# Performance work log

Hardware: AMD Instinct MI355X
Metric: run time of the kernel (lower is better)

## Reference

```python
import jax, jax.numpy as jnp
import numpy as np

N_NODES = 100000
N_EDGES = 1600000
D = 64
N_LAYERS = 3  # in -> h1 -> h2 -> out
LN_EPS = 1e-5


def setup_inputs() -> dict:
    key = jax.random.key(0)
    ks = jax.random.split(key, 4)
    scale = 1.0 / np.sqrt(D)
    vert_features = jax.random.normal(ks[0], (N_NODES, D), dtype=jnp.float32)
    edges = jax.random.randint(ks[1], (N_EDGES, 2), 0, N_NODES, dtype=jnp.int64)
    W0 = jax.random.normal(ks[2], (N_LAYERS, D, D), dtype=jnp.float32) * scale
    W1 = jax.random.normal(ks[3], (N_LAYERS, D, D), dtype=jnp.float32) * scale
    b0 = jnp.zeros((N_LAYERS, D), dtype=jnp.float32)
    b1 = jnp.zeros((N_LAYERS, D), dtype=jnp.float32)
    ln_gamma = jnp.ones((N_LAYERS - 1, D), dtype=jnp.float32)
    ln_beta = jnp.zeros((N_LAYERS - 1, D), dtype=jnp.float32)
    return {"vert_features": vert_features, "edges": edges, "W0": W0, "b0": b0,
            "W1": W1, "b1": b1, "ln_gamma": ln_gamma, "ln_beta": ln_beta}


def _graph_conv(h, src, dst, deg, W0l, b0l, W1l, b1l):
    # messages from every vertex, then undirected neighbor-mean aggregation
    msg = h @ W1l + b1l                                   # [N, D]
    idx = jnp.concatenate([dst, src])                     # both directions
    val = jnp.concatenate([msg[src], msg[dst]])           # [2E, D] gather
    agg = jax.ops.segment_sum(val, idx, num_segments=N_NODES)
    agg = agg / deg[:, None]                              # normalize=True
    return h @ W0l + b0l + agg


def _layer_norm(x, gamma, beta):
    mu = jnp.mean(x, axis=-1, keepdims=True)
    var = jnp.mean(jnp.square(x - mu), axis=-1, keepdims=True)
    return (x - mu) * jax.lax.rsqrt(var + LN_EPS) * gamma + beta


def reference(vert_features, edges, W0, b0, W1, b1, ln_gamma, ln_beta):
    src = edges[:, 0]
    dst = edges[:, 1]
    idx = jnp.concatenate([dst, src])
    deg = jax.ops.segment_sum(jnp.ones((2 * N_EDGES,), jnp.float32), idx,
                              num_segments=N_NODES)
    deg = jnp.maximum(deg, 1.0)
    h = vert_features
    for l in range(N_LAYERS - 1):
        h = _graph_conv(h, src, dst, deg, W0[l], b0[l], W1[l], b1[l])
        h = _layer_norm(h, ln_gamma[l], ln_beta[l])
        h = jax.nn.relu(h)
    h = _graph_conv(h, src, dst, deg, W0[-1], b0[-1], W1[-1], b1[-1])
    return h
```

## Files before the change

kernel.cpp:

```cpp
#include <hip/hip_runtime.h>
#include <hip/hip_bf16.h>

constexpr int D_ = 64;
constexpr int NN = 100000;
constexpr int NE = 1600000;
constexpr int RB = 8;

constexpr int BUCK_SH = 7;
constexpr int NBUCK = (NN + 127) >> BUCK_SH;
constexpr int NB1 = 256;
constexpr int NQ4 = NE / 4;
constexpr int QPB = (NQ4 + NB1 - 1) / NB1;
constexpr int SCN = NBUCK * NB1;
constexpr int SCB = (SCN + 1023) / 1024;

__global__ __launch_bounds__(256) void k_s1count(const int* __restrict__ edges,
                                                 int* __restrict__ cnts) {
  __shared__ int hist[NBUCK];
  for (int i = threadIdx.x; i < NBUCK; i += 256) hist[i] = 0;
  __syncthreads();
  const int q0 = blockIdx.x * QPB;
  const int q1 = min(q0 + QPB, NQ4);
  for (int q = q0 + (int)threadIdx.x; q < q1; q += 256) {
    const int4* ep = reinterpret_cast<const int4*>(edges + 8 * q);
    int4 a = ep[0], b = ep[1];
    atomicAdd(&hist[a.x >> BUCK_SH], 1);
    atomicAdd(&hist[a.y >> BUCK_SH], 1);
    atomicAdd(&hist[a.z >> BUCK_SH], 1);
    atomicAdd(&hist[a.w >> BUCK_SH], 1);
    atomicAdd(&hist[b.x >> BUCK_SH], 1);
    atomicAdd(&hist[b.y >> BUCK_SH], 1);
    atomicAdd(&hist[b.z >> BUCK_SH], 1);
    atomicAdd(&hist[b.w >> BUCK_SH], 1);
  }
  __syncthreads();
  for (int i = threadIdx.x; i < NBUCK; i += 256)
    cnts[i * NB1 + blockIdx.x] = hist[i];
}

__global__ __launch_bounds__(1024) void k_scanA(const int* __restrict__ cnt,
                                                int* __restrict__ oscan,
                                                int* __restrict__ bsum, int n) {
  __shared__ int sd[1024];
  const int tid = threadIdx.x;
  const int i = blockIdx.x * 1024 + tid;
  int v = (i < n) ? cnt[i] : 0;
  sd[tid] = v;
  __syncthreads();
  for (int off = 1; off < 1024; off <<= 1) {
    int t = (tid >= off) ? sd[tid - off] : 0;
    __syncthreads();
    sd[tid] += t;
    __syncthreads();
  }
  if (i < n) oscan[i] = sd[tid] - v;
  if (tid == 1023) bsum[blockIdx.x] = sd[1023];
}

__global__ __launch_bounds__(256) void k_scanB(int* __restrict__ bsum, int nb) {
  __shared__ int sd[256];
  const int tid = threadIdx.x;
  int v = (tid < nb) ? bsum[tid] : 0;
  sd[tid] = v;
  __syncthreads();
  for (int off = 1; off < 256; off <<= 1) {
    int t = (tid >= off) ? sd[tid - off] : 0;
    __syncthreads();
    sd[tid] += t;
    __syncthreads();
  }
  if (tid < nb) bsum[tid] = sd[tid] - v;
}

__global__ __launch_bounds__(256) void k_scanC(int* __restrict__ oscan,
                                               const int* __restrict__ bsum, int n) {
  int i = blockIdx.x * 256 + threadIdx.x;
  if (i < n) oscan[i] += bsum[i >> 10];
}

__global__ __launch_bounds__(256) void k_s1scatter(const int* __restrict__ edges,
                                                   const int* __restrict__ sscan,
                                                   unsigned* __restrict__ items) {
  __shared__ int cur[NBUCK];
  for (int i = threadIdx.x; i < NBUCK; i += 256)
    cur[i] = sscan[i * NB1 + blockIdx.x];
  __syncthreads();
  const int q0 = blockIdx.x * QPB;
  const int q1 = min(q0 + QPB, NQ4);
  for (int q = q0 + (int)threadIdx.x; q < q1; q += 256) {
    const int4* ep = reinterpret_cast<const int4*>(edges + 8 * q);
    int4 a = ep[0], b = ep[1];
    int p;
    p = atomicAdd(&cur[a.y >> BUCK_SH], 1); items[p] = ((unsigned)(a.y & 127) << 17) | (unsigned)a.x;
    p = atomicAdd(&cur[a.x >> BUCK_SH], 1); items[p] = ((unsigned)(a.x & 127) << 17) | (unsigned)a.y;
    p = atomicAdd(&cur[a.w >> BUCK_SH], 1); items[p] = ((unsigned)(a.w & 127) << 17) | (unsigned)a.z;
    p = atomicAdd(&cur[a.z >> BUCK_SH], 1); items[p] = ((unsigned)(a.z & 127) << 17) | (unsigned)a.w;
    p = atomicAdd(&cur[b.y >> BUCK_SH], 1); items[p] = ((unsigned)(b.y & 127) << 17) | (unsigned)b.x;
    p = atomicAdd(&cur[b.x >> BUCK_SH], 1); items[p] = ((unsigned)(b.x & 127) << 17) | (unsigned)b.y;
    p = atomicAdd(&cur[b.w >> BUCK_SH], 1); items[p] = ((unsigned)(b.w & 127) << 17) | (unsigned)b.z;
    p = atomicAdd(&cur[b.z >> BUCK_SH], 1); items[p] = ((unsigned)(b.z & 127) << 17) | (unsigned)b.w;
  }
}

__global__ __launch_bounds__(256) void k_s2build(const unsigned* __restrict__ items,
                                                 const int* __restrict__ sscan,
                                                 int* __restrict__ offs,
                                                 int* __restrict__ nbr) {
  const int b = blockIdx.x;
  const int lo = b << BUCK_SH;
  __shared__ int hist[128], scn[128];
  __shared__ int sbase, send;
  if (threadIdx.x == 0) {
    sbase = sscan[b * NB1];
    send = (b + 1 < NBUCK) ? sscan[(b + 1) * NB1] : 2 * NE;
  }
  if (threadIdx.x < 128) hist[threadIdx.x] = 0;
  __syncthreads();
  const int i0 = sbase, i1 = send;
  for (int i = i0 + (int)threadIdx.x; i < i1; i += 256)
    atomicAdd(&hist[items[i] >> 17], 1);
  __syncthreads();
  if (threadIdx.x < 128) scn[threadIdx.x] = hist[threadIdx.x];
  __syncthreads();
  for (int off = 1; off < 128; off <<= 1) {
    int t = (threadIdx.x < 128 && (int)threadIdx.x >= off) ? scn[threadIdx.x - off] : 0;
    __syncthreads();
    if (threadIdx.x < 128) scn[threadIdx.x] += t;
    __syncthreads();
  }
  if (threadIdx.x < 128) {
    int node = lo + threadIdx.x;
    int ex = sbase + scn[threadIdx.x] - hist[threadIdx.x];
    if (node < NN) offs[node] = ex;
    hist[threadIdx.x] = ex;
  }
  __syncthreads();
  for (int i = i0 + (int)threadIdx.x; i < i1; i += 256) {
    unsigned it = items[i];
    int pos = atomicAdd(&hist[it >> 17], 1);
    nbr[pos] = (int)(it & 0x1FFFFu);
  }
  if (b == 0 && threadIdx.x == 0) offs[NN] = 2 * NE;
}

__device__ __forceinline__ void stage_w_pk(const float* __restrict__ W0,
                                           const float* __restrict__ W1,
                                           unsigned* wP) {
  for (int i = threadIdx.x; i < 4096; i += 256) {
    int k = i >> 6, j = i & 63;
    wP[j * 68 + k] = (__float_as_uint(W1[i]) & 0xffff0000u) |
                     (__float_as_uint(W0[i]) >> 16);
  }
}

__device__ __forceinline__ unsigned char f32_to_f8(float v) {
  return (unsigned char)(__builtin_amdgcn_cvt_pk_fp8_f32(v, v, 0, false) & 0xff);
}

#define ACC8(mvv)                                                   \
  do {                                                              \
    auto lo = __builtin_amdgcn_cvt_pk_f32_fp8((mvv), false);        \
    auto hi = __builtin_amdgcn_cvt_pk_f32_fp8((mvv), true);         \
    acc[0] += lo[0]; acc[1] += lo[1]; acc[2] += hi[0]; acc[3] += hi[1]; \
  } while (0)

__device__ __forceinline__ float gather_row_q8(const unsigned* __restrict__ msgu,
                                               const int* __restrict__ nbr,
                                               int n0, int n1, int q, int c,
                                               int lane) {
  float acc[4] = {0.0f, 0.0f, 0.0f, 0.0f};
  int jb = n0;
  if (jb + 32 <= n1) {
    int idx[8];
#pragma unroll
    for (int u = 0; u < 8; ++u) idx[u] = nbr[jb + 4 * u + q];
    for (;;) {
      unsigned mv[8];
#pragma unroll
      for (int u = 0; u < 8; ++u) mv[u] = msgu[(idx[u] << 4) + c];
      const int jn = jb + 32;
      const bool more = (jn + 32 <= n1);
      if (more) {
#pragma unroll
        for (int u = 0; u < 8; ++u) idx[u] = nbr[jn + 4 * u + q];
      }
#pragma unroll
      for (int u = 0; u < 8; ++u) ACC8(mv[u]);
      jb = jn;
      if (!more) break;
    }
  }
  if (jb + 16 <= n1) {
    int idx[4];
#pragma unroll
    for (int u = 0; u < 4; ++u) idx[u] = nbr[jb + 4 * u + q];
    unsigned mv[4];
#pragma unroll
    for (int u = 0; u < 4; ++u) mv[u] = msgu[(idx[u] << 4) + c];
#pragma unroll
    for (int u = 0; u < 4; ++u) ACC8(mv[u]);
    jb += 16;
  }
  if (jb + 8 <= n1) {
    int i0 = nbr[jb + q], i1 = nbr[jb + 4 + q];
    unsigned m0 = msgu[(i0 << 4) + c];
    unsigned m1 = msgu[(i1 << 4) + c];
    ACC8(m0);
    ACC8(m1);
    jb += 8;
  }
  if (jb < n1) {
    int i0 = nbr[min(jb + q, n1 - 1)];
    int i1 = nbr[min(jb + 4 + q, n1 - 1)];
    unsigned m0 = msgu[(i0 << 4) + c];
    unsigned m1 = msgu[(i1 << 4) + c];
    if (jb + q >= n1) m0 = 0u;
    if (jb + 4 + q >= n1) m1 = 0u;
    ACC8(m0);
    ACC8(m1);
  }
#pragma unroll
  for (int k = 0; k < 4; ++k) {
    acc[k] += __shfl_xor(acc[k], 16, 64);
    acc[k] += __shfl_xor(acc[k], 32, 64);
  }
  float t0 = __shfl(acc[0], lane >> 2, 64);
  float t1 = __shfl(acc[1], lane >> 2, 64);
  float t2 = __shfl(acc[2], lane >> 2, 64);
  float t3 = __shfl(acc[3], lane >> 2, 64);
  const int s = lane & 3;
  return (s == 0) ? t0 : ((s == 1) ? t1 : ((s == 2) ? t2 : t3));
}

__device__ __forceinline__ void gemm_batch(const unsigned* wP,
                                           const float* myrows, int lane,
                                           float bv0, float bv1,
                                           float* a0, float* a1) {
#pragma unroll
  for (int rr = 0; rr < RB; ++rr) { a0[rr] = bv0; a1[rr] = bv1; }
#pragma unroll 1
  for (int k4 = 0; k4 < 16; ++k4) {
    uint4 up = *reinterpret_cast<const uint4*>(&wP[lane * 68 + k4 * 4]);
    const float v0x = __uint_as_float(up.x << 16);
    const float v1x = __uint_as_float(up.x & 0xffff0000u);
    const float v0y = __uint_as_float(up.y << 16);
    const float v1y = __uint_as_float(up.y & 0xffff0000u);
    const float v0z = __uint_as_float(up.z << 16);
    const float v1z = __uint_as_float(up.z & 0xffff0000u);
    const float v0w = __uint_as_float(up.w << 16);
    const float v1w = __uint_as_float(up.w & 0xffff0000u);
#pragma unroll
    for (int rr = 0; rr < RB; ++rr) {
      float4 hv = *reinterpret_cast<const float4*>(&myrows[rr * 64 + k4 * 4]);
      a0[rr] = fmaf(hv.x, v0x, a0[rr]); a1[rr] = fmaf(hv.x, v1x, a1[rr]);
      a0[rr] = fmaf(hv.y, v0y, a0[rr]); a1[rr] = fmaf(hv.y, v1y, a1[rr]);
      a0[rr] = fmaf(hv.z, v0z, a0[rr]); a1[rr] = fmaf(hv.z, v1z, a1[rr]);
      a0[rr] = fmaf(hv.w, v0w, a0[rr]); a1[rr] = fmaf(hv.w, v1w, a1[rr]);
    }
  }
}

__global__ __launch_bounds__(256) void k_gemm2(
    const float* __restrict__ h, const float* __restrict__ W0,
    const float* __restrict__ b0, const float* __restrict__ W1,
    const float* __restrict__ b1, float* __restrict__ base,
    unsigned char* __restrict__ msg, int nrows) {
  __shared__ unsigned wP[64 * 68];
  __shared__ float rbuf[4][RB * 64];
  stage_w_pk(W0, W1, wP);
  __syncthreads();
  const int lane = threadIdx.x & 63;
  const int wv = threadIdx.x >> 6;
  const int wid = (blockIdx.x * 256 + threadIdx.x) >> 6;
  const int nw = (gridDim.x * 256) >> 6;
  const float bv0 = b0[lane], bv1 = b1[lane];
  float* myrows = rbuf[wv];

  const int chunk = (nrows + nw - 1) / nw;
  const int r0 = wid * chunk;
  const int r1 = min(r0 + chunk, nrows);
  if (r0 >= nrows) return;

  float st[RB];
#pragma unroll
  for (int rr = 0; rr < RB; ++rr) {
    int r = min(r0 + rr, nrows - 1);
    st[rr] = h[(size_t)r * 64 + lane];
  }
  for (int rb = r0; rb < r1; rb += RB) {
#pragma unroll
    for (int rr = 0; rr < RB; ++rr) myrows[rr * 64 + lane] = st[rr];
    const int nb = rb + RB;
    if (nb < r1) {
#pragma unroll
      for (int rr = 0; rr < RB; ++rr) {
        int r = min(nb + rr, nrows - 1);
        st[rr] = h[(size_t)r * 64 + lane];
      }
    }
    float a0[RB], a1[RB];
    gemm_batch(wP, myrows, lane, bv0, bv1, a0, a1);
#pragma unroll
    for (int rr = 0; rr < RB; ++rr) {
      int r = rb + rr;
      if (r < r1) {
        base[(size_t)r * 64 + lane] = a0[rr];
        msg[(size_t)r * 64 + lane] = f32_to_f8(a1[rr]);
      }
    }
  }
}

__global__ __launch_bounds__(256) void k_fused(
    float* __restrict__ base, const unsigned char* __restrict__ msgin,
    unsigned char* __restrict__ msgout,
    const int* __restrict__ offs, const int* __restrict__ nbr,
    const float* __restrict__ gamma, const float* __restrict__ beta,
    const float* __restrict__ W0n, const float* __restrict__ b0n,
    const float* __restrict__ W1n, const float* __restrict__ b1n, int nrows) {
  __shared__ unsigned wP[64 * 68];
  __shared__ float rbuf[4][RB * 64];
  stage_w_pk(W0n, W1n, wP);
  __syncthreads();
  const int lane = threadIdx.x & 63;
  const int wv = threadIdx.x >> 6;
  const int q = lane >> 4;
  const int c = lane & 15;
  const int wid = (blockIdx.x * 256 + threadIdx.x) >> 6;
  const int nw = (gridDim.x * 256) >> 6;
  const float gm = gamma[lane], bt = beta[lane];
  const float bv0 = b0n[lane], bv1 = b1n[lane];
  float* myrows = rbuf[wv];
  const unsigned* msgu = reinterpret_cast<const unsigned*>(msgin);

  const int chunk = (nrows + nw - 1) / nw;
  const int r0 = wid * chunk;
  const int r1 = min(r0 + chunk, nrows);
  if (r0 >= nrows) return;

  for (int rb = r0; rb < r1; rb += RB) {
#pragma unroll 1
    for (int rr = 0; rr < RB; ++rr) {
      int r = rb + rr;
      if (r >= r1) break;
      const int n0 = offs[r], n1 = offs[r + 1];
      const float bval = base[(size_t)r * 64 + lane];
      float ag = gather_row_q8(msgu, nbr, n0, n1, q, c, lane);
      const float rdeg = 1.0f / fmaxf((float)(n1 - n0), 1.0f);
      float val = fmaf(ag, rdeg, bval);
      float s = val, s2 = val * val;
#pragma unroll
      for (int off = 32; off > 0; off >>= 1) {
        s += __shfl_xor(s, off, 64);
        s2 += __shfl_xor(s2, off, 64);
      }
      const float mu = s * (1.0f / 64.0f);
      const float var = fmaxf(s2 * (1.0f / 64.0f) - mu * mu, 0.0f);
      const float dv = val - mu;
      val = fmaxf(fmaf(dv * rsqrtf(var + 1e-5f), gm, bt), 0.0f);
      myrows[rr * 64 + lane] = val;
    }
    float a0[RB], a1[RB];
    gemm_batch(wP, myrows, lane, bv0, bv1, a0, a1);
#pragma unroll
    for (int rr = 0; rr < RB; ++rr) {
      int r = rb + rr;
      if (r < r1) {
        base[(size_t)r * 64 + lane] = a0[rr];
        msgout[(size_t)r * 64 + lane] = f32_to_f8(a1[rr]);
      }
    }
  }
}

__global__ __launch_bounds__(256) void k_aggF(
    float* __restrict__ base, const unsigned char* __restrict__ msg,
    const int* __restrict__ offs, const int* __restrict__ nbr, int nrows) {
  const int lane = threadIdx.x & 63;
  const int q = lane >> 4;
  const int c = lane & 15;
  const int wid = (blockIdx.x * 256 + threadIdx.x) >> 6;
  const int nw = (gridDim.x * 256) >> 6;
  const unsigned* msgu = reinterpret_cast<const unsigned*>(msg);
  for (int r = wid; r < nrows; r += nw) {
    const int n0 = offs[r], n1 = offs[r + 1];
    const float bval = base[(size_t)r * 64 + lane];
    float ag = gather_row_q8(msgu, nbr, n0, n1, q, c, lane);
    const float rdeg = 1.0f / fmaxf((float)(n1 - n0), 1.0f);
    base[(size_t)r * 64 + lane] = fmaf(ag, rdeg, bval);
  }
}

extern "C" void kernel_launch(void* const* d_in, const int* in_sizes, int n_in,
                              void* d_out, int out_size, void* d_ws, size_t ws_size,
                              hipStream_t stream) {
  const float* vert = (const float*)d_in[0];
  const int* edges = (const int*)d_in[1];
  const float* W0 = (const float*)d_in[2];
  const float* b0 = (const float*)d_in[3];
  const float* W1 = (const float*)d_in[4];
  const float* b1 = (const float*)d_in[5];
  const float* lng = (const float*)d_in[6];
  const float* lnb = (const float*)d_in[7];
  float* base = (float*)d_out;

  const size_t NBR_B = (size_t)2 * NE * 4;
  const size_t MSG_B = (size_t)NN * 64;
  int* nbr = (int*)d_ws;
  char* creg = (char*)d_ws + NBR_B;
  unsigned* items = (unsigned*)creg;
  unsigned char* msgA = (unsigned char*)creg;
  unsigned char* msgB = (unsigned char*)(creg + MSG_B);
  int* offs = (int*)(creg + NBR_B);
  int* cnts = (int*)d_out;
  int* sscan = cnts + SCN;
  int* bsum = sscan + SCN;

  k_s1count<<<NB1, 256, 0, stream>>>(edges, cnts);
  k_scanA<<<SCB, 1024, 0, stream>>>(cnts, sscan, bsum, SCN);
  k_scanB<<<1, 256, 0, stream>>>(bsum, SCB);
  k_scanC<<<(SCN + 255) / 256, 256, 0, stream>>>(sscan, bsum, SCN);
  k_s1scatter<<<NB1, 256, 0, stream>>>(edges, sscan, items);
  k_s2build<<<NBUCK, 256, 0, stream>>>(items, sscan, offs, nbr);

  const int GG = 1536;
  const int GF = 1536;
  const int GA = 2048;

  k_gemm2<<<GG, 256, 0, stream>>>(vert, W0, b0, W1, b1, base, msgA, NN);
  k_fused<<<GF, 256, 0, stream>>>(base, msgA, msgB, offs, nbr,
                                  lng, lnb, W0 + 4096, b0 + 64,
                                  W1 + 4096, b1 + 64, NN);
  k_fused<<<GF, 256, 0, stream>>>(base, msgB, msgA, offs, nbr,
                                  lng + 64, lnb + 64, W0 + 8192, b0 + 128,
                                  W1 + 8192, b1 + 128, NN);
  k_aggF<<<GA, 256, 0, stream>>>(base, msgA, offs, nbr, NN);
}
```

Measured before the change: 373.6 us.

## Gather neighbor messages for four rows at once per wavefront

Replaces the single-row neighbor gather with a gather4 routine. It walks the adjacency lists of four rows together, issuing up to 16 independent index and message loads per step. The goal is more memory-level parallelism, to hide the latency of the random fp8 message gathers in both the fused LN+GEMM kernel and the final aggregation kernel. The final aggregation kernel also switches from strided to contiguous per-wave row chunks. In exchange, each group loops until its highest-degree row is done, with masked loads, and register pressure rises from the 4x4 accumulators.

```diff
diff --git a/kernel.cpp b/kernel.cpp
--- a/kernel.cpp
+++ b/kernel.cpp
@@ -157,79 +157,72 @@
   return (unsigned char)(__builtin_amdgcn_cvt_pk_fp8_f32(v, v, 0, false) & 0xff);
 }
 
-#define ACC8(mvv)                                                   \
-  do {                                                              \
-    auto lo = __builtin_amdgcn_cvt_pk_f32_fp8((mvv), false);        \
-    auto hi = __builtin_amdgcn_cvt_pk_f32_fp8((mvv), true);         \
-    acc[0] += lo[0]; acc[1] += lo[1]; acc[2] += hi[0]; acc[3] += hi[1]; \
-  } while (0)
-
-__device__ __forceinline__ float gather_row_q8(const unsigned* __restrict__ msgu,
-                                               const int* __restrict__ nbr,
-                                               int n0, int n1, int q, int c,
-                                               int lane) {
-  float acc[4] = {0.0f, 0.0f, 0.0f, 0.0f};
-  int jb = n0;
-  if (jb + 32 <= n1) {
-    int idx[8];
-#pragma unroll
-    for (int u = 0; u < 8; ++u) idx[u] = nbr[jb + 4 * u + q];
-    for (;;) {
-      unsigned mv[8];
-#pragma unroll
-      for (int u = 0; u < 8; ++u) mv[u] = msgu[(idx[u] << 4) + c];
-      const int jn = jb + 32;
-      const bool more = (jn + 32 <= n1);
-      if (more) {
-#pragma unroll
-        for (int u = 0; u < 8; ++u) idx[u] = nbr[jn + 4 * u + q];
-      }
-#pragma unroll
-      for (int u = 0; u < 8; ++u) ACC8(mv[u]);
-      jb = jn;
-      if (!more) break;
-    }
-  }
-  if (jb + 16 <= n1) {
-    int idx[4];
-#pragma unroll
-    for (int u = 0; u < 4; ++u) idx[u] = nbr[jb + 4 * u + q];
-    unsigned mv[4];
-#pragma unroll
-    for (int u = 0; u < 4; ++u) mv[u] = msgu[(idx[u] << 4) + c];
-#pragma unroll
-    for (int u = 0; u < 4; ++u) ACC8(mv[u]);
-    jb += 16;
-  }
-  if (jb + 8 <= n1) {
-    int i0 = nbr[jb + q], i1 = nbr[jb + 4 + q];
-    unsigned m0 = msgu[(i0 << 4) + c];
-    unsigned m1 = msgu[(i1 << 4) + c];
-    ACC8(m0);
-    ACC8(m1);
-    jb += 8;
-  }
-  if (jb < n1) {
-    int i0 = nbr[min(jb + q, n1 - 1)];
-    int i1 = nbr[min(jb + 4 + q, n1 - 1)];
-    unsigned m0 = msgu[(i0 << 4) + c];
-    unsigned m1 = msgu[(i1 << 4) + c];
-    if (jb + q >= n1) m0 = 0u;
-    if (jb + 4 + q >= n1) m1 = 0u;
-    ACC8(m0);
-    ACC8(m1);
-  }
-#pragma unroll
-  for (int k = 0; k < 4; ++k) {
-    acc[k] += __shfl_xor(acc[k], 16, 64);
-    acc[k] += __shfl_xor(acc[k], 32, 64);
-  }
-  float t0 = __shfl(acc[0], lane >> 2, 64);
-  float t1 = __shfl(acc[1], lane >> 2, 64);
-  float t2 = __shfl(acc[2], lane >> 2, 64);
-  float t3 = __shfl(acc[3], lane >> 2, 64);
-  const int s = lane & 3;
-  return (s == 0) ? t0 : ((s == 1) ? t1 : ((s == 2) ? t2 : t3));
+__device__ __forceinline__ void gather4(const unsigned* __restrict__ msgu,
+                                        const int* __restrict__ nbr,
+                                        const int* __restrict__ offs,
+                                        int rbase, int rclamp,
+                                        int q, int c, int lane,
+                                        float* __restrict__ val,
+                                        float* __restrict__ rdeg) {
+  int n1[4], jb[4];
+#pragma unroll
+  for (int i = 0; i < 4; ++i) {
+    int r = min(rbase + i, rclamp);
+    jb[i] = offs[r];
+    n1[i] = offs[r + 1];
+    rdeg[i] = 1.0f / fmaxf((float)(n1[i] - jb[i]), 1.0f);
+  }
+  float acc[4][4];
+#pragma unroll
+  for (int i = 0; i < 4; ++i)
+#pragma unroll
+    for (int k = 0; k < 4; ++k) acc[i][k] = 0.0f;
+  bool any = (jb[0] < n1[0]) | (jb[1] < n1[1]) | (jb[2] < n1[2]) | (jb[3] < n1[3]);
+  while (any) {
+    unsigned mv[4][4];
+#pragma unroll
+    for (int i = 0; i < 4; ++i) {
+      if (jb[i] < n1[i]) {
+#pragma unroll
+        for (int u = 0; u < 4; ++u) {
+          int id = nbr[min(jb[i] + 4 * u + q, n1[i] - 1)];
+          mv[i][u] = msgu[(id << 4) + c];
+        }
+      }
+    }
+#pragma unroll
+    for (int i = 0; i < 4; ++i) {
+      if (jb[i] < n1[i]) {
+#pragma unroll
+        for (int u = 0; u < 4; ++u) {
+          unsigned m = (jb[i] + 4 * u + q < n1[i]) ? mv[i][u] : 0u;
+          auto lo = __builtin_amdgcn_cvt_pk_f32_fp8(m, false);
+          auto hi = __builtin_amdgcn_cvt_pk_f32_fp8(m, true);
+          acc[i][0] += lo[0]; acc[i][1] += lo[1];
+          acc[i][2] += hi[0]; acc[i][3] += hi[1];
+        }
+      }
+    }
+    any = false;
+#pragma unroll
+    for (int i = 0; i < 4; ++i) { jb[i] += 16; any = any | (jb[i] < n1[i]); }
+  }
+#pragma unroll
+  for (int i = 0; i < 4; ++i)
+#pragma unroll
+    for (int k = 0; k < 4; ++k) {
+      acc[i][k] += __shfl_xor(acc[i][k], 16, 64);
+      acc[i][k] += __shfl_xor(acc[i][k], 32, 64);
+    }
+#pragma unroll
+  for (int i = 0; i < 4; ++i) {
+    float t0 = __shfl(acc[i][0], lane >> 2, 64);
+    float t1 = __shfl(acc[i][1], lane >> 2, 64);
+    float t2 = __shfl(acc[i][2], lane >> 2, 64);
+    float t3 = __shfl(acc[i][3], lane >> 2, 64);
+    const int s = lane & 3;
+    val[i] = (s == 0) ? t0 : ((s == 1) ? t1 : ((s == 2) ? t2 : t3));
+  }
 }
 
 __device__ __forceinline__ void gemm_batch(const unsigned* wP,
@@ -339,26 +332,37 @@
   if (r0 >= nrows) return;
 
   for (int rb = r0; rb < r1; rb += RB) {
-#pragma unroll 1
-    for (int rr = 0; rr < RB; ++rr) {
-      int r = rb + rr;
-      if (r >= r1) break;
-      const int n0 = offs[r], n1 = offs[r + 1];
-      const float bval = base[(size_t)r * 64 + lane];
-      float ag = gather_row_q8(msgu, nbr, n0, n1, q, c, lane);
-      const float rdeg = 1.0f / fmaxf((float)(n1 - n0), 1.0f);
-      float val = fmaf(ag, rdeg, bval);
-      float s = val, s2 = val * val;
+#pragma unroll
+    for (int g = 0; g < 2; ++g) {
+      const int gb = rb + g * 4;
+      float bv4[4];
+#pragma unroll
+      for (int i = 0; i < 4; ++i)
+        bv4[i] = base[(size_t)min(gb + i, nrows - 1) * 64 + lane];
+      float v4[4], rd4[4];
+      gather4(msgu, nbr, offs, gb, nrows - 1, q, c, lane, v4, rd4);
+      float vals[4];
+#pragma unroll
+      for (int i = 0; i < 4; ++i) vals[i] = fmaf(v4[i], rd4[i], bv4[i]);
+      float sA[4], sB[4];
+#pragma unroll
+      for (int i = 0; i < 4; ++i) { sA[i] = vals[i]; sB[i] = vals[i] * vals[i]; }
 #pragma unroll
       for (int off = 32; off > 0; off >>= 1) {
-        s += __shfl_xor(s, off, 64);
-        s2 += __shfl_xor(s2, off, 64);
-      }
-      const float mu = s * (1.0f / 64.0f);
-      const float var = fmaxf(s2 * (1.0f / 64.0f) - mu * mu, 0.0f);
-      const float dv = val - mu;
-      val = fmaxf(fmaf(dv * rsqrtf(var + 1e-5f), gm, bt), 0.0f);
-      myrows[rr * 64 + lane] = val;
+#pragma unroll
+        for (int i = 0; i < 4; ++i) {
+          sA[i] += __shfl_xor(sA[i], off, 64);
+          sB[i] += __shfl_xor(sB[i], off, 64);
+        }
+      }
+#pragma unroll
+      for (int i = 0; i < 4; ++i) {
+        const float mu = sA[i] * (1.0f / 64.0f);
+        const float var = fmaxf(sB[i] * (1.0f / 64.0f) - mu * mu, 0.0f);
+        const float dv = vals[i] - mu;
+        const float o = fmaxf(fmaf(dv * rsqrtf(var + 1e-5f), gm, bt), 0.0f);
+        myrows[(g * 4 + i) * 64 + lane] = o;
+      }
     }
     float a0[RB], a1[RB];
     gemm_batch(wP, myrows, lane, bv0, bv1, a0, a1);
@@ -382,12 +386,23 @@
   const int wid = (blockIdx.x * 256 + threadIdx.x) >> 6;
   const int nw = (gridDim.x * 256) >> 6;
   const unsigned* msgu = reinterpret_cast<const unsigned*>(msg);
-  for (int r = wid; r < nrows; r += nw) {
-    const int n0 = offs[r], n1 = offs[r + 1];
-    const float bval = base[(size_t)r * 64 + lane];
-    float ag = gather_row_q8(msgu, nbr, n0, n1, q, c, lane);
-    const float rdeg = 1.0f / fmaxf((float)(n1 - n0), 1.0f);
-    base[(size_t)r * 64 + lane] = fmaf(ag, rdeg, bval);
+  const int chunk = (((nrows + nw - 1) / nw) + 3) & ~3;
+  const int r0 = wid * chunk;
+  const int r1 = min(r0 + chunk, nrows);
+  if (r0 >= nrows) return;
+  for (int rb = r0; rb < r1; rb += 4) {
+    float bv4[4];
+#pragma unroll
+    for (int i = 0; i < 4; ++i)
+      bv4[i] = base[(size_t)min(rb + i, nrows - 1) * 64 + lane];
+    float v4[4], rd4[4];
+    gather4(msgu, nbr, offs, rb, nrows - 1, q, c, lane, v4, rd4);
+#pragma unroll
+    for (int i = 0; i < 4; ++i) {
+      int r = rb + i;
+      if (r < r1)
+        base[(size_t)r * 64 + lane] = fmaf(v4[i], rd4[i], bv4[i]);
+    }
   }
 }
 
```

Result: slower. 452.5 us (+21.1%).

## Split fused aggregate+LN+GEMM kernel into separate aggregate-LN and GEMM kernels

Applied to the files above, without the earlier changes.

Replaces the fused per-layer kernel (gather aggregation, layernorm, relu, then a shared-memory GEMM for the next layer) with two kernels: a gather+layernorm kernel that writes an fp32 hidden buffer, followed by the existing standalone GEMM kernel. The aim is to decouple the irregular, latency-bound gather from the GEMM so each kernel gets its own occupancy and work split. The fused kernel also carried shared-memory weight staging and a contiguous per-wave row chunking. The split costs an extra 25.6 MB round trip for the hidden activations and two more launches per run.

```diff
diff --git a/kernel.cpp b/kernel.cpp
--- a/kernel.cpp
+++ b/kernel.cpp
@@ -311,65 +311,35 @@
   }
 }
 
-__global__ __launch_bounds__(256) void k_fused(
-    float* __restrict__ base, const unsigned char* __restrict__ msgin,
-    unsigned char* __restrict__ msgout,
+__global__ __launch_bounds__(256) void k_aggLN(
+    const float* __restrict__ base, const unsigned char* __restrict__ msg,
     const int* __restrict__ offs, const int* __restrict__ nbr,
     const float* __restrict__ gamma, const float* __restrict__ beta,
-    const float* __restrict__ W0n, const float* __restrict__ b0n,
-    const float* __restrict__ W1n, const float* __restrict__ b1n, int nrows) {
-  __shared__ unsigned wP[64 * 68];
-  __shared__ float rbuf[4][RB * 64];
-  stage_w_pk(W0n, W1n, wP);
-  __syncthreads();
+    float* __restrict__ hout, int nrows) {
   const int lane = threadIdx.x & 63;
-  const int wv = threadIdx.x >> 6;
   const int q = lane >> 4;
   const int c = lane & 15;
   const int wid = (blockIdx.x * 256 + threadIdx.x) >> 6;
   const int nw = (gridDim.x * 256) >> 6;
   const float gm = gamma[lane], bt = beta[lane];
-  const float bv0 = b0n[lane], bv1 = b1n[lane];
-  float* myrows = rbuf[wv];
-  const unsigned* msgu = reinterpret_cast<const unsigned*>(msgin);
-
-  const int chunk = (nrows + nw - 1) / nw;
-  const int r0 = wid * chunk;
-  const int r1 = min(r0 + chunk, nrows);
-  if (r0 >= nrows) return;
-
-  for (int rb = r0; rb < r1; rb += RB) {
-#pragma unroll 1
-    for (int rr = 0; rr < RB; ++rr) {
-      int r = rb + rr;
-      if (r >= r1) break;
-      const int n0 = offs[r], n1 = offs[r + 1];
-      const float bval = base[(size_t)r * 64 + lane];
-      float ag = gather_row_q8(msgu, nbr, n0, n1, q, c, lane);
-      const float rdeg = 1.0f / fmaxf((float)(n1 - n0), 1.0f);
-      float val = fmaf(ag, rdeg, bval);
-      float s = val, s2 = val * val;
-#pragma unroll
-      for (int off = 32; off > 0; off >>= 1) {
-        s += __shfl_xor(s, off, 64);
-        s2 += __shfl_xor(s2, off, 64);
-      }
-      const float mu = s * (1.0f / 64.0f);
-      const float var = fmaxf(s2 * (1.0f / 64.0f) - mu * mu, 0.0f);
-      const float dv = val - mu;
-      val = fmaxf(fmaf(dv * rsqrtf(var + 1e-5f), gm, bt), 0.0f);
-      myrows[rr * 64 + lane] = val;
+  const unsigned* msgu = reinterpret_cast<const unsigned*>(msg);
+  for (int r = wid; r < nrows; r += nw) {
+    const int n0 = offs[r], n1 = offs[r + 1];
+    const float bval = base[(size_t)r * 64 + lane];
+    float ag = gather_row_q8(msgu, nbr, n0, n1, q, c, lane);
+    const float rdeg = 1.0f / fmaxf((float)(n1 - n0), 1.0f);
+    float val = fmaf(ag, rdeg, bval);
+    float s = val, s2 = val * val;
+#pragma unroll
+    for (int off = 32; off > 0; off >>= 1) {
+      s += __shfl_xor(s, off, 64);
+      s2 += __shfl_xor(s2, off, 64);
     }
-    float a0[RB], a1[RB];
-    gemm_batch(wP, myrows, lane, bv0, bv1, a0, a1);
-#pragma unroll
-    for (int rr = 0; rr < RB; ++rr) {
-      int r = rb + rr;
-      if (r < r1) {
-        base[(size_t)r * 64 + lane] = a0[rr];
-        msgout[(size_t)r * 64 + lane] = f32_to_f8(a1[rr]);
-      }
-    }
+    const float mu = s * (1.0f / 64.0f);
+    const float var = fmaxf(s2 * (1.0f / 64.0f) - mu * mu, 0.0f);
+    const float dv = val - mu;
+    val = fmaxf(fmaf(dv * rsqrtf(var + 1e-5f), gm, bt), 0.0f);
+    hout[(size_t)r * 64 + lane] = val;
   }
 }
 
@@ -406,12 +376,14 @@
 
   const size_t NBR_B = (size_t)2 * NE * 4;
   const size_t MSG_B = (size_t)NN * 64;
+  const size_t HB = (size_t)NN * 64 * 4;
   int* nbr = (int*)d_ws;
   char* creg = (char*)d_ws + NBR_B;
   unsigned* items = (unsigned*)creg;
   unsigned char* msgA = (unsigned char*)creg;
   unsigned char* msgB = (unsigned char*)(creg + MSG_B);
-  int* offs = (int*)(creg + NBR_B);
+  float* hbuf = (float*)(creg + NBR_B);
+  int* offs = (int*)((char*)hbuf + HB);
   int* cnts = (int*)d_out;
   int* sscan = cnts + SCN;
   int* bsum = sscan + SCN;
@@ -424,15 +396,15 @@
   k_s2build<<<NBUCK, 256, 0, stream>>>(items, sscan, offs, nbr);
 
   const int GG = 1536;
-  const int GF = 1536;
   const int GA = 2048;
 
   k_gemm2<<<GG, 256, 0, stream>>>(vert, W0, b0, W1, b1, base, msgA, NN);
-  k_fused<<<GF, 256, 0, stream>>>(base, msgA, msgB, offs, nbr,
-                                  lng, lnb, W0 + 4096, b0 + 64,
-                                  W1 + 4096, b1 + 64, NN);
-  k_fused<<<GF, 256, 0, stream>>>(base, msgB, msgA, offs, nbr,
-                                  lng + 64, lnb + 64, W0 + 8192, b0 + 128,
-                                  W1 + 8192, b1 + 128, NN);
+  k_aggLN<<<GA, 256, 0, stream>>>(base, msgA, offs, nbr, lng, lnb, hbuf, NN);
+  k_gemm2<<<GG, 256, 0, stream>>>(hbuf, W0 + 4096, b0 + 64,
+                                  W1 + 4096, b1 + 64, base, msgB, NN);
+  k_aggLN<<<GA, 256, 0, stream>>>(base, msgB, offs, nbr, lng + 64, lnb + 64,
+                                  hbuf, NN);
+  k_gemm2<<<GG, 256, 0, stream>>>(hbuf, W0 + 8192, b0 + 128,
+                                  W1 + 8192, b1 + 128, base, msgA, NN);
   k_aggF<<<GA, 256, 0, stream>>>(base, msgA, offs, nbr, NN);
 }
```

New measurement: 372.6 us. No clear change (-0.3%).
